# Kernel tuning notes

Measured on AMD Instinct MI355X. Metric: run time of the kernel, lower is better.

The kernel has to match this reference:

```python
import jax, jax.numpy as jnp
import numpy as np

NUM_NODES = 4904
EMBED_DIM = 300
NUM_CLASSES = 14


def setup_inputs() -> dict:
    key = jax.random.key(0)
    k1, k2, k3, k4, k5, k6, k7, k8 = jax.random.split(key, 8)
    B, L, K = 128, 512, 8
    master_nodes = jax.random.randint(k1, (B, L), 0, NUM_NODES + 1)
    slave_nodes = jax.random.randint(k2, (B, L, K), 0, NUM_NODES + 1)
    slave_edges = jax.random.randint(k3, (B, L, K), 0, NUM_NODES * NUM_NODES + 1)
    # Embedding tables (padding_idx=0 -> zero row)
    R = jax.random.normal(k4, (NUM_NODES + 1, EMBED_DIM), dtype=jnp.float32)
    R = R.at[0].set(0.0)
    E = jax.random.normal(k5, (NUM_NODES * NUM_NODES + 1, 1), dtype=jnp.float32)
    E = E.at[0].set(0.0)
    N = jax.random.normal(k6, (NUM_NODES + 1, 1), dtype=jnp.float32)
    N = N.at[0].set(0.0)
    # fc: Linear(300 -> 14)
    bound = 1.0 / np.sqrt(EMBED_DIM)
    W = jax.random.uniform(k7, (NUM_CLASSES, EMBED_DIM), minval=-bound, maxval=bound, dtype=jnp.float32)
    b = jax.random.uniform(k8, (NUM_CLASSES,), minval=-bound, maxval=bound, dtype=jnp.float32)
    return {"master_nodes": master_nodes, "slave_nodes": slave_nodes,
            "slave_edges": slave_edges, "R": R, "E": E, "N": N, "W": W, "b": b}


def reference(master_nodes, slave_nodes, slave_edges, R, E, N, W, b):
    Rn = R[master_nodes]          # [B, L, D]
    Ra = R[slave_nodes]           # [B, L, K, D]
    Ean = E[slave_edges]          # [B, L, K, 1]
    Mn = jnp.max(Ra * Ean, axis=2)  # [B, L, D] max-pool over neighbors
    Nn = N[master_nodes]          # [B, L, 1] gate
    x = (1.0 - Nn) * Mn + Nn * Rn  # [B, L, D]
    x = jnp.sum(x, axis=1)         # [B, D]
    h = jax.nn.relu(x @ W.T + b)   # [B, C]
    # Dropout is identity in eval mode; softmax over classes (dim=1)
    return jax.nn.softmax(h, axis=1)
```

## Files before the change

### kernel.cpp

```cpp
#include <hip/hip_runtime.h>
#include <hip/hip_fp16.h>
#include <math.h>

#define BB 128
#define LL 512
#define KK 8
#define DD 300
#define D2 150
#define CC 14
#define L_PER_BLOCK 8
#define UNROLL 4

#define R_H2_ELEMS ((4905 * 300) / 2)
#define R_F4_ELEMS ((4905 * 300) / 4)
#define REC_INTS 20

typedef _Float16 h2 __attribute__((ext_vector_type(2)));

__global__ __launch_bounds__(256) void prep(
    const float4* __restrict__ R4, const int* __restrict__ edges,
    const float* __restrict__ E, const int* __restrict__ master,
    const float* __restrict__ N, const int* __restrict__ slaves,
    h2* __restrict__ R16, int* __restrict__ rec, float* __restrict__ X)
{
    const int i = blockIdx.x * 256 + threadIdx.x;

    if (i < R_F4_ELEMS) {
        const float4 f = R4[i];
        h2 a; a.x = (_Float16)f.x; a.y = (_Float16)f.y;
        h2 b; b.x = (_Float16)f.z; b.y = (_Float16)f.w;
        R16[2 * i]     = a;
        R16[2 * i + 1] = b;
    }
    if (i < BB * LL * KK) {
        const int bl = i >> 3, k = i & 7;
        rec[bl * REC_INTS + 2 + 2 * k] = slaves[i] * D2;
        const _Float16 ev = (_Float16)E[edges[i]];
        h2 p; p.x = ev; p.y = ev;
        rec[bl * REC_INTS + 3 + 2 * k] = __builtin_bit_cast(int, p);
    }
    if (i < BB * LL) {
        const int m = master[i];
        rec[i * REC_INTS]     = m * D2;
        rec[i * REC_INTS + 1] = __float_as_int(N[m]);
    }
    if (i < BB * DD) X[i] = 0.f;
}

__global__ __launch_bounds__(192) void gnn_agg(
    const int4* __restrict__ rec4, const h2* __restrict__ Rv,
    float* __restrict__ X)
{
    const int b  = blockIdx.x;
    const int lc = blockIdx.y;
    const int t  = threadIdx.x;
    const bool act = (t < D2);

    float accx = 0.f, accy = 0.f;
    const int bl_base = b * LL + lc * L_PER_BLOCK;

    for (int lg = 0; lg < L_PER_BLOCK; lg += UNROLL) {
        int   offm[UNROLL], offs[UNROLL][KK], eb[UNROLL][KK];
        float nn[UNROLL];

#pragma unroll
        for (int u = 0; u < UNROLL; ++u) {
            const int4* r = rec4 + (long)(bl_base + lg + u) * (REC_INTS / 4);
            const int4 q0 = r[0];
            const int4 q1 = r[1];
            const int4 q2 = r[2];
            const int4 q3 = r[3];
            const int4 q4 = r[4];
            offm[u] = q0.x;            nn[u]    = __int_as_float(q0.y);
            offs[u][0] = q0.z;         eb[u][0] = q0.w;
            offs[u][1] = q1.x;         eb[u][1] = q1.y;
            offs[u][2] = q1.z;         eb[u][2] = q1.w;
            offs[u][3] = q2.x;         eb[u][3] = q2.y;
            offs[u][4] = q2.z;         eb[u][4] = q2.w;
            offs[u][5] = q3.x;         eb[u][5] = q3.y;
            offs[u][6] = q3.z;         eb[u][6] = q3.w;
            offs[u][7] = q4.x;         eb[u][7] = q4.y;
        }

        if (act) {
            h2 r[UNROLL][KK], rm[UNROLL];
#pragma unroll
            for (int u = 0; u < UNROLL; ++u) {
#pragma unroll
                for (int k = 0; k < KK; ++k) r[u][k] = (Rv + offs[u][k])[t];
            }
#pragma unroll
            for (int u = 0; u < UNROLL; ++u) rm[u] = (Rv + offm[u])[t];

#pragma unroll
            for (int u = 0; u < UNROLL; ++u) {
                h2 mx = r[u][0] * __builtin_bit_cast(h2, eb[u][0]);
#pragma unroll
                for (int k = 1; k < KK; ++k)
                    mx = __builtin_elementwise_max(
                        mx, r[u][k] * __builtin_bit_cast(h2, eb[u][k]));
                const float n = nn[u], a = 1.f - n;
                accx = fmaf(a, (float)mx.x, fmaf(n, (float)rm[u].x, accx));
                accy = fmaf(a, (float)mx.y, fmaf(n, (float)rm[u].y, accy));
            }
        }
    }
    if (act) {
        atomicAdd(&X[b * DD + 2*t],     accx);
        atomicAdd(&X[b * DD + 2*t + 1], accy);
    }
}

__global__ __launch_bounds__(256) void fc_softmax(
    const float* __restrict__ X, const float* __restrict__ W,
    const float* __restrict__ bias, float* __restrict__ out)
{
    const int b = blockIdx.x;
    const int t = threadIdx.x;
    const int c = t >> 4;
    const int j = t & 15;
    __shared__ float h[CC];

    if (c < CC) {
        float acc = 0.f;
        const float* x = X + b * DD;
        const float* w = W + c * DD;
        for (int d = j; d < DD; d += 16) acc += x[d] * w[d];
#pragma unroll
        for (int off = 8; off > 0; off >>= 1) acc += __shfl_down(acc, off, 16);
        if (j == 0) h[c] = fmaxf(acc + bias[c], 0.f);
    }
    __syncthreads();
    if (t < CC) {
        float mx = -INFINITY;
#pragma unroll
        for (int i = 0; i < CC; ++i) mx = fmaxf(mx, h[i]);
        float s = 0.f;
#pragma unroll
        for (int i = 0; i < CC; ++i) s += expf(h[i] - mx);
        out[b * CC + t] = expf(h[t] - mx) / s;
    }
}

extern "C" void kernel_launch(void* const* d_in, const int* in_sizes, int n_in,
                              void* d_out, int out_size, void* d_ws, size_t ws_size,
                              hipStream_t stream) {
    const int*   master = (const int*)d_in[0];
    const int*   slaves = (const int*)d_in[1];
    const int*   edges  = (const int*)d_in[2];
    const float* R      = (const float*)d_in[3];
    const float* E      = (const float*)d_in[4];
    const float* N      = (const float*)d_in[5];
    const float* W      = (const float*)d_in[6];
    const float* bias   = (const float*)d_in[7];
    float* out = (float*)d_out;

    char* ws = (char*)d_ws;
    h2*    R16 = (h2*)ws;
    float* X   = (float*)(ws + 2943104);
    int*   rec = (int*)(ws + 2943104 + 153600);

    prep<<<(BB * LL * KK) / 256, 256, 0, stream>>>(
        (const float4*)R, edges, E, master, N, slaves, R16, rec, X);

    dim3 grid(BB, LL / L_PER_BLOCK);
    gnn_agg<<<grid, 192, 0, stream>>>((const int4*)rec, R16, X);

    fc_softmax<<<BB, 256, 0, stream>>>(X, W, bias, out);
}
```

Measured before the change: 192.1 us.

## Fuse index/edge gather into aggregation kernel, drop packed record buffer

Removes the prep-stage construction of a packed per-(b,l) record array and instead has gnn_agg read master/slave indices directly and gather edge weights and gates into shared memory per block. This eliminates a full write and re-read of the record buffer and shrinks the prep grid to only the R conversion. In exchange each block does an extra barrier and scattered E lookups inside the main kernel, and slave indices are loaded as scalar ints rather than packed int4s.

After: 189.5 us. Within noise of the previous version (-1.3%).

```diff
diff --git a/kernel.cpp b/kernel.cpp
--- a/kernel.cpp
+++ b/kernel.cpp
@@ -11,20 +11,14 @@
 #define L_PER_BLOCK 8
 #define UNROLL 4
 
-#define R_H2_ELEMS ((4905 * 300) / 2)
 #define R_F4_ELEMS ((4905 * 300) / 4)
-#define REC_INTS 20
 
 typedef _Float16 h2 __attribute__((ext_vector_type(2)));
 
 __global__ __launch_bounds__(256) void prep(
-    const float4* __restrict__ R4, const int* __restrict__ edges,
-    const float* __restrict__ E, const int* __restrict__ master,
-    const float* __restrict__ N, const int* __restrict__ slaves,
-    h2* __restrict__ R16, int* __restrict__ rec, float* __restrict__ X)
+    const float4* __restrict__ R4, h2* __restrict__ R16, float* __restrict__ X)
 {
     const int i = blockIdx.x * 256 + threadIdx.x;
-
     if (i < R_F4_ELEMS) {
         const float4 f = R4[i];
         h2 a; a.x = (_Float16)f.x; a.y = (_Float16)f.y;
@@ -32,54 +26,51 @@
         R16[2 * i]     = a;
         R16[2 * i + 1] = b;
     }
-    if (i < BB * LL * KK) {
-        const int bl = i >> 3, k = i & 7;
-        rec[bl * REC_INTS + 2 + 2 * k] = slaves[i] * D2;
-        const _Float16 ev = (_Float16)E[edges[i]];
-        h2 p; p.x = ev; p.y = ev;
-        rec[bl * REC_INTS + 3 + 2 * k] = __builtin_bit_cast(int, p);
-    }
-    if (i < BB * LL) {
-        const int m = master[i];
-        rec[i * REC_INTS]     = m * D2;
-        rec[i * REC_INTS + 1] = __float_as_int(N[m]);
-    }
     if (i < BB * DD) X[i] = 0.f;
 }
 
 __global__ __launch_bounds__(192) void gnn_agg(
-    const int4* __restrict__ rec4, const h2* __restrict__ Rv,
+    const int* __restrict__ master, const int* __restrict__ slaves,
+    const int* __restrict__ edges, const float* __restrict__ E,
+    const float* __restrict__ N, const h2* __restrict__ Rv,
     float* __restrict__ X)
 {
     const int b  = blockIdx.x;
     const int lc = blockIdx.y;
     const int t  = threadIdx.x;
     const bool act = (t < D2);
+    const int bl_base = b * LL + lc * L_PER_BLOCK;
+
+    __shared__ __align__(16) int ebuf[L_PER_BLOCK * KK];
+    __shared__ float nnbuf[L_PER_BLOCK];
+
+    if (t < L_PER_BLOCK * KK) {
+        const _Float16 ev = (_Float16)E[edges[bl_base * KK + t]];
+        h2 p; p.x = ev; p.y = ev;
+        ebuf[t] = __builtin_bit_cast(int, p);
+    } else if (t < L_PER_BLOCK * KK + L_PER_BLOCK) {
+        const int l = t - L_PER_BLOCK * KK;
+        nnbuf[l] = N[master[bl_base + l]];
+    }
+    __syncthreads();
 
     float accx = 0.f, accy = 0.f;
-    const int bl_base = b * LL + lc * L_PER_BLOCK;
 
     for (int lg = 0; lg < L_PER_BLOCK; lg += UNROLL) {
-        int   offm[UNROLL], offs[UNROLL][KK], eb[UNROLL][KK];
+        int   offm[UNROLL], offs[UNROLL][KK];
+        int4  ea[UNROLL], eb2[UNROLL];
         float nn[UNROLL];
 
 #pragma unroll
         for (int u = 0; u < UNROLL; ++u) {
-            const int4* r = rec4 + (long)(bl_base + lg + u) * (REC_INTS / 4);
-            const int4 q0 = r[0];
-            const int4 q1 = r[1];
-            const int4 q2 = r[2];
-            const int4 q3 = r[3];
-            const int4 q4 = r[4];
-            offm[u] = q0.x;            nn[u]    = __int_as_float(q0.y);
-            offs[u][0] = q0.z;         eb[u][0] = q0.w;
-            offs[u][1] = q1.x;         eb[u][1] = q1.y;
-            offs[u][2] = q1.z;         eb[u][2] = q1.w;
-            offs[u][3] = q2.x;         eb[u][3] = q2.y;
-            offs[u][4] = q2.z;         eb[u][4] = q2.w;
-            offs[u][5] = q3.x;         eb[u][5] = q3.y;
-            offs[u][6] = q3.z;         eb[u][6] = q3.w;
-            offs[u][7] = q4.x;         eb[u][7] = q4.y;
+            const int bl = bl_base + lg + u;
+            offm[u] = master[bl] * D2;
+#pragma unroll
+            for (int k = 0; k < KK; ++k)
+                offs[u][k] = slaves[bl * KK + k] * D2;
+            ea[u]  = *(const int4*)&ebuf[(lg + u) * KK];
+            eb2[u] = *(const int4*)&ebuf[(lg + u) * KK + 4];
+            nn[u]  = nnbuf[lg + u];
         }
 
         if (act) {
@@ -94,11 +85,13 @@
 
 #pragma unroll
             for (int u = 0; u < UNROLL; ++u) {
-                h2 mx = r[u][0] * __builtin_bit_cast(h2, eb[u][0]);
+                const int ev[KK] = { ea[u].x, ea[u].y, ea[u].z, ea[u].w,
+                                     eb2[u].x, eb2[u].y, eb2[u].z, eb2[u].w };
+                h2 mx = r[u][0] * __builtin_bit_cast(h2, ev[0]);
 #pragma unroll
                 for (int k = 1; k < KK; ++k)
                     mx = __builtin_elementwise_max(
-                        mx, r[u][k] * __builtin_bit_cast(h2, eb[u][k]));
+                        mx, r[u][k] * __builtin_bit_cast(h2, ev[k]));
                 const float n = nn[u], a = 1.f - n;
                 accx = fmaf(a, (float)mx.x, fmaf(n, (float)rm[u].x, accx));
                 accy = fmaf(a, (float)mx.y, fmaf(n, (float)rm[u].y, accy));
@@ -158,13 +151,12 @@
     char* ws = (char*)d_ws;
     h2*    R16 = (h2*)ws;
     float* X   = (float*)(ws + 2943104);
-    int*   rec = (int*)(ws + 2943104 + 153600);
 
-    prep<<<(BB * LL * KK) / 256, 256, 0, stream>>>(
-        (const float4*)R, edges, E, master, N, slaves, R16, rec, X);
+    prep<<<(R_F4_ELEMS + 255) / 256, 256, 0, stream>>>(
+        (const float4*)R, R16, X);
 
     dim3 grid(BB, LL / L_PER_BLOCK);
-    gnn_agg<<<grid, 192, 0, stream>>>((const int4*)rec, R16, X);
+    gnn_agg<<<grid, 192, 0, stream>>>(master, slaves, edges, E, N, R16, X);
 
     fc_softmax<<<BB, 256, 0, stream>>>(X, W, bias, out);
 }
```
